# Optimization experiments

Hardware: AMD Instinct MI355X
Metric: run time of the kernel (lower is better)

Reference implementation:

```python
import jax, jax.numpy as jnp
import numpy as np

B = 262144      # batch (many robot-timestep samples)
IN_LEN = 32     # input_len
S = 64          # internal_state_len
M = 32          # message_len
P = 4           # num_ports
H = 100         # hidden_layer_size
L = 50          # lstm_hidden_size
O = 16          # output_len


def _linear_init(key, out_f, in_f):
    # torch.nn.Linear default init: U(-1/sqrt(in_f), 1/sqrt(in_f)) for W and b
    kw, kb = jax.random.split(key)
    bound = 1.0 / np.sqrt(in_f)
    W = jax.random.uniform(kw, (out_f, in_f), jnp.float32, -bound, bound)
    b = jax.random.uniform(kb, (out_f,), jnp.float32, -bound, bound)
    return W, b


def setup_inputs() -> dict:
    key = jax.random.key(0)
    ks = jax.random.split(key, 20)
    obs = jax.random.normal(ks[0], (B, IN_LEN), jnp.float32)
    messages_in = jax.random.normal(ks[1], (P, B, M), jnp.float32)
    h_lstm = jax.random.normal(ks[2], (B, L), jnp.float32)
    c_lstm = jax.random.normal(ks[3], (B, L), jnp.float32)

    W_in, b_in = _linear_init(ks[4], S, IN_LEN)
    # per-port message MLPs, stacked on a leading port axis
    msg1 = [_linear_init(jax.random.fold_in(ks[5], p), H, S) for p in range(P)]
    msg2 = [_linear_init(jax.random.fold_in(ks[6], p), M, H) for p in range(P)]
    msg_W1 = jnp.stack([w for w, _ in msg1])  # [P, H, S]
    msg_b1 = jnp.stack([b for _, b in msg1])  # [P, H]
    msg_W2 = jnp.stack([w for w, _ in msg2])  # [P, M, H]
    msg_b2 = jnp.stack([b for _, b in msg2])  # [P, M]

    # LSTMCell(S + M*P -> L); torch gate order i, f, g, o; init U(-1/sqrt(L), 1/sqrt(L))
    bl = 1.0 / np.sqrt(L)
    W_ih = jax.random.uniform(ks[7], (4 * L, S + M * P), jnp.float32, -bl, bl)
    W_hh = jax.random.uniform(ks[8], (4 * L, L), jnp.float32, -bl, bl)
    b_ih = jax.random.uniform(ks[9], (4 * L,), jnp.float32, -bl, bl)
    b_hh = jax.random.uniform(ks[10], (4 * L,), jnp.float32, -bl, bl)

    W_u1, b_u1 = _linear_init(ks[11], H, L)
    W_u2, b_u2 = _linear_init(ks[12], H, H)
    W_u3, b_u3 = _linear_init(ks[13], S, H)
    W_mu, b_mu = _linear_init(ks[14], O, S)
    W_var, b_var = _linear_init(ks[15], O, S)
    max_logvar = jnp.ones((1, O), jnp.float32) / 2.0
    min_logvar = -jnp.ones((1, O), jnp.float32) * 10.0

    return dict(obs=obs, messages_in=messages_in, h_lstm=h_lstm, c_lstm=c_lstm,
                W_in=W_in, b_in=b_in, msg_W1=msg_W1, msg_b1=msg_b1,
                msg_W2=msg_W2, msg_b2=msg_b2, W_ih=W_ih, W_hh=W_hh,
                b_ih=b_ih, b_hh=b_hh, W_u1=W_u1, b_u1=b_u1, W_u2=W_u2,
                b_u2=b_u2, W_u3=W_u3, b_u3=b_u3, W_mu=W_mu, b_mu=b_mu,
                W_var=W_var, b_var=b_var, max_logvar=max_logvar,
                min_logvar=min_logvar)


def reference(obs, messages_in, h_lstm, c_lstm, W_in, b_in, msg_W1, msg_b1,
              msg_W2, msg_b2, W_ih, W_hh, b_ih, b_hh, W_u1, b_u1, W_u2, b_u2,
              W_u3, b_u3, W_mu, b_mu, W_var, b_var, max_logvar, min_logvar):
    # run_input_function
    x = jax.nn.relu(obs @ W_in.T + b_in)                       # [B, S]

    # compute_messages_out_function: batched over ports (all ports occupied)
    m1 = jax.nn.relu(jnp.einsum('bs,phs->pbh', x, msg_W1) + msg_b1[:, None, :])
    msgs_out = jnp.einsum('pbh,pmh->pbm', m1, msg_W2) + msg_b2[:, None, :]  # [P, B, M]

    # compute_aggregation_function: concat incoming messages along feature dim
    agg = jnp.transpose(messages_in, (1, 0, 2)).reshape(obs.shape[0], -1)  # [B, P*M]
    h_mbar = jnp.concatenate([x, agg], axis=-1)                # [B, S + P*M]

    # status_update_function: one LSTMCell step (torch gate order i, f, g, o)
    gates = h_mbar @ W_ih.T + b_ih + h_lstm @ W_hh.T + b_hh    # [B, 4L]
    i, f, g, o = jnp.split(gates, 4, axis=-1)
    c_new = jax.nn.sigmoid(f) * c_lstm + jax.nn.sigmoid(i) * jnp.tanh(g)
    h_new = jax.nn.sigmoid(o) * jnp.tanh(c_new)                # [B, L]
    h2 = jax.nn.relu(h_new @ W_u1.T + b_u1)
    h2 = jax.nn.relu(h2 @ W_u2.T + b_u2)
    h2 = h2 @ W_u3.T + b_u3                                    # new internal state [B, S]

    # compute_output_function with soft logvar clamping
    mu = h2 @ W_mu.T + b_mu                                    # [B, O]
    logvar = h2 @ W_var.T + b_var
    logvar = max_logvar - jax.nn.softplus(max_logvar - logvar)
    logvar = min_logvar + jax.nn.softplus(logvar - min_logvar)
    var = jnp.exp(logvar)

    msgs_flat = jnp.transpose(msgs_out, (1, 0, 2)).reshape(obs.shape[0], -1)  # [B, P*M]
    # concat all outputs: mu(16) var(16) msgs(128) h2(64) h_new(50) c_new(50) = 324
    return jnp.concatenate([mu, var, msgs_flat, h2, h_new, c_new], axis=-1)
```

## Files before the change

kernel.cpp:

```cpp
#include <hip/hip_runtime.h>

typedef __bf16 bf16_t;
typedef __bf16 bf16x8 __attribute__((ext_vector_type(8)));
typedef float f32x4 __attribute__((ext_vector_type(4)));

#define B_TOTAL 262144
#define OUTC 324
#define ROWS 64

#define OFF_WIN   0
#define OFF_WG    2048
#define OFF_WM1   67584
#define OFF_WM2   96256
#define OFF_WU1   112640
#define OFF_WU2   119808
#define OFF_WU3   134144
#define OFF_WMV2  142336
#define BF16_TOTAL 145920

__global__ void prep_kernel(const float* W_in, const float* msg_W1, const float* msg_W2,
                            const float* W_ih, const float* W_hh, const float* b_ih, const float* b_hh,
                            const float* W_u1, const float* W_u2, const float* W_u3, const float* b_u3f,
                            const float* W_mu, const float* W_var, const float* b_mu, const float* b_var,
                            bf16_t* wb, float* bg, float* bmv) {
  int tid = blockIdx.x * blockDim.x + threadIdx.x;
  int nth = gridDim.x * blockDim.x;
  for (int i = tid; i < 2048; i += nth) wb[OFF_WIN + i] = (bf16_t)W_in[i];
  for (int i = tid; i < 65536; i += nth) {
    int n = i >> 8, k = i & 255;
    int g = n >> 6, j = n & 63;
    float v = 0.f;
    if (j < 50) {
      int r = g * 50 + j;
      if (k < 192) v = W_ih[r * 192 + k];
      else if (k < 242) v = W_hh[r * 50 + (k - 192)];
    }
    wb[OFF_WG + i] = (bf16_t)v;
  }
  for (int i = tid; i < 256; i += nth) {
    int g = i >> 6, j = i & 63;
    bg[i] = (j < 50) ? (b_ih[g * 50 + j] + b_hh[g * 50 + j]) : 0.f;
  }
  for (int i = tid; i < 4 * 112 * 64; i += nth) {
    int p = i / (112 * 64); int rem = i % (112 * 64); int n = rem >> 6, k = rem & 63;
    wb[OFF_WM1 + i] = (bf16_t)((n < 100) ? msg_W1[(p * 100 + n) * 64 + k] : 0.f);
  }
  for (int i = tid; i < 4 * 32 * 128; i += nth) {
    int p = i / (32 * 128); int rem = i % (32 * 128); int n = rem >> 7, k = rem & 127;
    wb[OFF_WM2 + i] = (bf16_t)((k < 100) ? msg_W2[(p * 32 + n) * 100 + k] : 0.f);
  }
  for (int i = tid; i < 112 * 64; i += nth) {
    int n = i >> 6, k = i & 63;
    wb[OFF_WU1 + i] = (bf16_t)((n < 100 && k < 50) ? W_u1[n * 50 + k] : 0.f);
  }
  for (int i = tid; i < 112 * 128; i += nth) {
    int n = i >> 7, k = i & 127;
    wb[OFF_WU2 + i] = (bf16_t)((n < 100 && k < 100) ? W_u2[n * 100 + k] : 0.f);
  }
  for (int i = tid; i < 64 * 128; i += nth) {
    int n = i >> 7, k = i & 127;
    wb[OFF_WU3 + i] = (bf16_t)((k < 100) ? W_u3[n * 100 + k] : 0.f);
  }
  for (int i = tid; i < 32 * 112; i += nth) {
    int o = i / 112, h = i % 112;
    float v = 0.f;
    if (h < 100) {
      const float* wrow = (o < 16) ? (W_mu + o * 64) : (W_var + (o - 16) * 64);
      for (int s = 0; s < 64; s++) v += wrow[s] * W_u3[s * 100 + h];
    }
    wb[OFF_WMV2 + i] = (bf16_t)v;
  }
  for (int i = tid; i < 32; i += nth) {
    int o = i;
    const float* wrow = (o < 16) ? (W_mu + o * 64) : (W_var + (o - 16) * 64);
    float v = (o < 16) ? b_mu[o] : b_var[o - 16];
    for (int s = 0; s < 64; s++) v += wrow[s] * b_u3f[s];
    bmv[o] = v;
  }
}

#define MFMA(a, b, c) __builtin_amdgcn_mfma_f32_16x16x32_bf16((a), (b), (c), 0, 0, 0)

__device__ __forceinline__ float frcp(float x) { return __builtin_amdgcn_rcpf(x); }
__device__ __forceinline__ float fsigmoid(float x) { return frcp(1.f + __expf(-x)); }
__device__ __forceinline__ float ftanh_f(float x) { return 1.f - 2.f * frcp(1.f + __expf(2.f * x)); }
__device__ __forceinline__ float fsoftplus(float x) { return (x > 15.f) ? x : __logf(1.f + __expf(x)); }

__device__ __forceinline__ bf16x8 cvt8(const float* __restrict__ p) {
  float4 v0 = *(const float4*)p;
  float4 v1 = *(const float4*)(p + 4);
  bf16x8 r;
  r[0] = (bf16_t)v0.x; r[1] = (bf16_t)v0.y; r[2] = (bf16_t)v0.z; r[3] = (bf16_t)v0.w;
  r[4] = (bf16_t)v1.x; r[5] = (bf16_t)v1.y; r[6] = (bf16_t)v1.z; r[7] = (bf16_t)v1.w;
  return r;
}

__device__ __forceinline__ void stage2(int p, const bf16x8 ax[4][2], bf16_t* dst,
                                       const bf16_t* __restrict__ wb,
                                       const float* __restrict__ msg_b1,
                                       int w, int lr, int kq) {
  for (int nt = w; nt < 7; nt += 4) {
    int nb = nt * 16;
    float bv = (nb + lr < 100) ? msg_b1[p * 100 + nb + lr] : 0.f;
    const bf16_t* Bp = wb + OFF_WM1 + p * 112 * 64 + (nb + lr) * 64 + kq * 8;
    bf16x8 b0 = *(const bf16x8*)Bp;
    bf16x8 b1 = *(const bf16x8*)(Bp + 32);
#pragma unroll
    for (int m = 0; m < 4; m++) {
      f32x4 acc = {bv, bv, bv, bv};
      acc = MFMA(ax[m][0], b0, acc);
      acc = MFMA(ax[m][1], b1, acc);
#pragma unroll
      for (int rr = 0; rr < 4; rr++)
        dst[(m * 16 + kq * 4 + rr) * 120 + nb + lr] = (bf16_t)fmaxf(acc[rr], 0.f);
    }
  }
}

__device__ __forceinline__ void stage3(int p, const bf16_t* src,
                                       const bf16_t* __restrict__ wb,
                                       const float* __restrict__ msg_b2,
                                       float* __restrict__ out,
                                       int row0, int w, int lr, int kq) {
  int nb = (w & 1) * 16;
  float bv = msg_b2[p * 32 + nb + lr];
  const bf16_t* Bp = wb + OFF_WM2 + p * 32 * 128 + (nb + lr) * 128 + kq * 8;
  bf16x8 b[4];
#pragma unroll
  for (int c = 0; c < 4; c++) b[c] = *(const bf16x8*)(Bp + c * 32);
#pragma unroll
  for (int mi = 0; mi < 2; mi++) {
    int m = (w >> 1) + mi * 2;
    f32x4 acc = {bv, bv, bv, bv};
#pragma unroll
    for (int c = 0; c < 4; c++) {
      bf16x8 a;
      if (c < 3) {
        a = *(const bf16x8*)(src + (m * 16 + lr) * 120 + c * 32 + kq * 8);
      } else {
        bf16x8 z = {};
        a = (kq < 2) ? *(const bf16x8*)(src + (m * 16 + lr) * 120 + 96 + kq * 8) : z;
      }
      acc = MFMA(a, b[c], acc);
    }
#pragma unroll
    for (int rr = 0; rr < 4; rr++) {
      size_t row = row0 + m * 16 + kq * 4 + rr;
      out[row * OUTC + 32 + p * 32 + nb + lr] = acc[rr];
    }
  }
}

__global__ __launch_bounds__(256, 3) void fused_kernel(
    const float* __restrict__ obs, const float* __restrict__ msg_in,
    const float* __restrict__ h_lstm, const float* __restrict__ c_lstm,
    const float* __restrict__ b_in, const float* __restrict__ msg_b1,
    const float* __restrict__ msg_b2, const float* __restrict__ b_u1,
    const float* __restrict__ b_u2, const float* __restrict__ b_u3,
    const float* __restrict__ maxlv, const float* __restrict__ minlv,
    const bf16_t* __restrict__ wb, const float* __restrict__ bg,
    const float* __restrict__ bmv, float* __restrict__ out) {
  __shared__ __align__(16) bf16_t xh[ROWS * 136];
  __shared__ __align__(16) bf16_t tA[ROWS * 120];
  __shared__ __align__(16) bf16_t tB[ROWS * 120];

  const int tid = threadIdx.x;
  const int row0 = blockIdx.x * ROWS;
  const int lane = tid & 63;
  const int w = tid >> 6;
  const int lr = lane & 15;
  const int kq = lane >> 4;

  {
    int r = tid >> 2, c0 = (tid & 3) * 16;
    const float* s = h_lstm + (size_t)(row0 + r) * 50;
    bf16x8 pk0, pk1;
#pragma unroll
    for (int q = 0; q < 8; q++) {
      int c = c0 + q;
      pk0[q] = (bf16_t)((c < 50) ? s[c] : 0.f);
    }
#pragma unroll
    for (int q = 0; q < 8; q++) {
      int c = c0 + 8 + q;
      pk1[q] = (bf16_t)((c < 50) ? s[c] : 0.f);
    }
    *(bf16x8*)(xh + r * 136 + 64 + c0) = pk0;
    *(bf16x8*)(xh + r * 136 + 64 + c0 + 8) = pk1;
  }

  {
    int nb = w * 16;
    float bv = b_in[nb + lr];
    bf16x8 b0 = *(const bf16x8*)(wb + OFF_WIN + (nb + lr) * 32 + kq * 8);
#pragma unroll
    for (int m = 0; m < 4; m++) {
      bf16x8 a0 = cvt8(obs + (size_t)(row0 + m * 16 + lr) * 32 + kq * 8);
      f32x4 acc = {bv, bv, bv, bv};
      acc = MFMA(a0, b0, acc);
#pragma unroll
      for (int rr = 0; rr < 4; rr++)
        xh[(m * 16 + kq * 4 + rr) * 136 + nb + lr] = (bf16_t)fmaxf(acc[rr], 0.f);
    }
  }
  __syncthreads();

  bf16x8 ax[4][2];
#pragma unroll
  for (int m = 0; m < 4; m++)
#pragma unroll
    for (int k = 0; k < 2; k++)
      ax[m][k] = *(const bf16x8*)(xh + (m * 16 + lr) * 136 + k * 32 + kq * 8);

  stage2(0, ax, tA, wb, msg_b1, w, lr, kq);
  __syncthreads();

  stage3(0, tA, wb, msg_b2, out, row0, w, lr, kq);
  stage2(1, ax, tB, wb, msg_b1, w, lr, kq);
  __syncthreads();
  stage3(1, tB, wb, msg_b2, out, row0, w, lr, kq);
  stage2(2, ax, tA, wb, msg_b1, w, lr, kq);
  __syncthreads();
  stage3(2, tA, wb, msg_b2, out, row0, w, lr, kq);
  stage2(3, ax, tB, wb, msg_b1, w, lr, kq);
  __syncthreads();

  {
    const int mt = w >> 1, jh = w & 1;
    const int jbase = jh * 32;
    bf16x8 m_pre[4][2];
#pragma unroll
    for (int p = 0; p < 4; p++)
#pragma unroll
      for (int ms = 0; ms < 2; ms++)
        m_pre[p][ms] = cvt8(msg_in + ((size_t)p * B_TOTAL + row0 + mt * 32 + ms * 16 + lr) * 32 + kq * 8);
    float c_pre[2][2][4];
#pragma unroll
    for (int s = 0; s < 2; s++) {
      int j = jbase + s * 16 + lr;
#pragma unroll
      for (int ms = 0; ms < 2; ms++)
#pragma unroll
        for (int rr = 0; rr < 4; rr++) {
          size_t row = row0 + mt * 32 + ms * 16 + kq * 4 + rr;
          c_pre[s][ms][rr] = (j < 50) ? c_lstm[row * 50 + j] : 0.f;
        }
    }

    stage3(3, tB, wb, msg_b2, out, row0, w, lr, kq);

    f32x4 acc[4][2][2];
#pragma unroll
    for (int g = 0; g < 4; g++)
#pragma unroll
      for (int s = 0; s < 2; s++) {
        float bb = bg[g * 64 + jbase + s * 16 + lr];
        f32x4 bi = {bb, bb, bb, bb};
        acc[g][s][0] = bi;
        acc[g][s][1] = bi;
      }
#pragma unroll
    for (int c = 0; c < 8; c++) {
      bf16x8 a[2];
#pragma unroll
      for (int ms = 0; ms < 2; ms++) {
        int row = mt * 32 + ms * 16 + lr;
        if (c < 2) {
          a[ms] = *(const bf16x8*)(xh + row * 136 + c * 32 + kq * 8);
        } else if (c < 6) {
          a[ms] = m_pre[c - 2][ms];
        } else {
          a[ms] = *(const bf16x8*)(xh + row * 136 + 64 + (c - 6) * 32 + kq * 8);
        }
      }
#pragma unroll
      for (int g = 0; g < 4; g++)
#pragma unroll
        for (int s = 0; s < 2; s++) {
          bf16x8 bfrag = *(const bf16x8*)(wb + OFF_WG +
              (size_t)(g * 64 + jbase + s * 16 + lr) * 256 + c * 32 + kq * 8);
          acc[g][s][0] = MFMA(a[0], bfrag, acc[g][s][0]);
          acc[g][s][1] = MFMA(a[1], bfrag, acc[g][s][1]);
        }
    }
#pragma unroll
    for (int s = 0; s < 2; s++) {
      int j = jbase + s * 16 + lr;
#pragma unroll
      for (int ms = 0; ms < 2; ms++) {
        int rbase = mt * 32 + ms * 16 + kq * 4;
#pragma unroll
        for (int rr = 0; rr < 4; rr++) {
          int lrow = rbase + rr;
          size_t row = row0 + lrow;
          float si = fsigmoid(acc[0][s][ms][rr]);
          float sf = fsigmoid(acc[1][s][ms][rr]);
          float gv = ftanh_f(acc[2][s][ms][rr]);
          float so = fsigmoid(acc[3][s][ms][rr]);
          float cn = sf * c_pre[s][ms][rr] + si * gv;
          float hv = so * ftanh_f(cn);
          if (j < 50) {
            out[row * OUTC + 274 + j] = cn;
            out[row * OUTC + 224 + j] = hv;
          }
          tA[lrow * 120 + j] = (bf16_t)((j < 50) ? hv : 0.f);
        }
      }
    }
  }
  __syncthreads();

  for (int nt = w; nt < 7; nt += 4) {
    int nb = nt * 16;
    float bv = (nb + lr < 100) ? b_u1[nb + lr] : 0.f;
    const bf16_t* Bp = wb + OFF_WU1 + (nb + lr) * 64 + kq * 8;
    bf16x8 b0 = *(const bf16x8*)Bp;
    bf16x8 b1 = *(const bf16x8*)(Bp + 32);
#pragma unroll
    for (int m = 0; m < 4; m++) {
      bf16x8 a0 = *(const bf16x8*)(tA + (m * 16 + lr) * 120 + kq * 8);
      bf16x8 a1 = *(const bf16x8*)(tA + (m * 16 + lr) * 120 + kq * 8 + 32);
      f32x4 acc = {bv, bv, bv, bv};
      acc = MFMA(a0, b0, acc);
      acc = MFMA(a1, b1, acc);
#pragma unroll
      for (int rr = 0; rr < 4; rr++)
        tB[(m * 16 + kq * 4 + rr) * 120 + nb + lr] = (bf16_t)fmaxf(acc[rr], 0.f);
    }
  }
  __syncthreads();

  for (int nt = w; nt < 7; nt += 4) {
    int nb = nt * 16;
    float bv = (nb + lr < 100) ? b_u2[nb + lr] : 0.f;
    const bf16_t* Bp = wb + OFF_WU2 + (nb + lr) * 128 + kq * 8;
    bf16x8 b[4];
#pragma unroll
    for (int c = 0; c < 4; c++) b[c] = *(const bf16x8*)(Bp + c * 32);
#pragma unroll
    for (int m = 0; m < 4; m++) {
      f32x4 acc = {bv, bv, bv, bv};
#pragma unroll
      for (int c = 0; c < 4; c++) {
        bf16x8 a;
        if (c < 3) {
          a = *(const bf16x8*)(tB + (m * 16 + lr) * 120 + c * 32 + kq * 8);
        } else {
          bf16x8 z = {};
          a = (kq < 2) ? *(const bf16x8*)(tB + (m * 16 + lr) * 120 + 96 + kq * 8) : z;
        }
        acc = MFMA(a, b[c], acc);
      }
#pragma unroll
      for (int rr = 0; rr < 4; rr++)
        tA[(m * 16 + kq * 4 + rr) * 120 + nb + lr] = (bf16_t)fmaxf(acc[rr], 0.f);
    }
  }
  __syncthreads();

  {
    int nb = w * 16;
    float bv = b_u3[nb + lr];
    const bf16_t* Bp = wb + OFF_WU3 + (nb + lr) * 128 + kq * 8;
    bf16x8 b[4];
#pragma unroll
    for (int c = 0; c < 4; c++) b[c] = *(const bf16x8*)(Bp + c * 32);
#pragma unroll
    for (int m = 0; m < 4; m++) {
      f32x4 acc = {bv, bv, bv, bv};
#pragma unroll
      for (int c = 0; c < 4; c++) {
        bf16x8 a;
        if (c < 3) {
          a = *(const bf16x8*)(tA + (m * 16 + lr) * 120 + c * 32 + kq * 8);
        } else {
          bf16x8 z = {};
          a = (kq < 2) ? *(const bf16x8*)(tA + (m * 16 + lr) * 120 + 96 + kq * 8) : z;
        }
        acc = MFMA(a, b[c], acc);
      }
#pragma unroll
      for (int rr = 0; rr < 4; rr++) {
        size_t row = row0 + m * 16 + kq * 4 + rr;
        out[row * OUTC + 160 + nb + lr] = acc[rr];
      }
    }
  }

  {
    int t = w & 1;
    const bf16_t* Bp = wb + OFF_WMV2 + (t * 16 + lr) * 112 + kq * 8;
    bf16x8 b[4];
#pragma unroll
    for (int c = 0; c < 3; c++) b[c] = *(const bf16x8*)(Bp + c * 32);
    {
      bf16x8 z = {};
      b[3] = (kq < 2) ? *(const bf16x8*)(Bp + 96) : z;
    }
    float bv = bmv[t * 16 + lr];
    float mx = maxlv[lr], mn = minlv[lr];
#pragma unroll
    for (int mi = 0; mi < 2; mi++) {
      int m = (w >> 1) + mi * 2;
      f32x4 acc = {bv, bv, bv, bv};
#pragma unroll
      for (int c = 0; c < 4; c++) {
        bf16x8 a;
        if (c < 3) {
          a = *(const bf16x8*)(tA + (m * 16 + lr) * 120 + c * 32 + kq * 8);
        } else {
          bf16x8 z = {};
          a = (kq < 2) ? *(const bf16x8*)(tA + (m * 16 + lr) * 120 + 96 + kq * 8) : z;
        }
        acc = MFMA(a, b[c], acc);
      }
      if (t == 0) {
#pragma unroll
        for (int rr = 0; rr < 4; rr++) {
          size_t row = row0 + m * 16 + kq * 4 + rr;
          out[row * OUTC + lr] = acc[rr];
        }
      } else {
#pragma unroll
        for (int rr = 0; rr < 4; rr++) {
          size_t row = row0 + m * 16 + kq * 4 + rr;
          float lv = acc[rr];
          lv = mx - fsoftplus(mx - lv);
          lv = mn + fsoftplus(lv - mn);
          out[row * OUTC + 16 + lr] = __expf(lv);
        }
      }
    }
  }
}

extern "C" void kernel_launch(void* const* d_in, const int* in_sizes, int n_in,
                              void* d_out, int out_size, void* d_ws, size_t ws_size,
                              hipStream_t stream) {
  const float* obs   = (const float*)d_in[0];
  const float* msgs  = (const float*)d_in[1];
  const float* h_l   = (const float*)d_in[2];
  const float* c_l   = (const float*)d_in[3];
  const float* W_in  = (const float*)d_in[4];
  const float* b_in  = (const float*)d_in[5];
  const float* mW1   = (const float*)d_in[6];
  const float* mb1   = (const float*)d_in[7];
  const float* mW2   = (const float*)d_in[8];
  const float* mb2   = (const float*)d_in[9];
  const float* W_ih  = (const float*)d_in[10];
  const float* W_hh  = (const float*)d_in[11];
  const float* b_ih  = (const float*)d_in[12];
  const float* b_hh  = (const float*)d_in[13];
  const float* W_u1  = (const float*)d_in[14];
  const float* b_u1  = (const float*)d_in[15];
  const float* W_u2  = (const float*)d_in[16];
  const float* b_u2  = (const float*)d_in[17];
  const float* W_u3  = (const float*)d_in[18];
  const float* b_u3  = (const float*)d_in[19];
  const float* W_mu  = (const float*)d_in[20];
  const float* b_mu  = (const float*)d_in[21];
  const float* W_var = (const float*)d_in[22];
  const float* b_var = (const float*)d_in[23];
  const float* maxlv = (const float*)d_in[24];
  const float* minlv = (const float*)d_in[25];

  bf16_t* wb = (bf16_t*)d_ws;
  float* bg  = (float*)((char*)d_ws + (size_t)BF16_TOTAL * 2);
  float* bmv = bg + 256;

  prep_kernel<<<64, 256, 0, stream>>>(W_in, mW1, mW2, W_ih, W_hh, b_ih, b_hh,
                                      W_u1, W_u2, W_u3, b_u3, W_mu, W_var, b_mu, b_var,
                                      wb, bg, bmv);
  fused_kernel<<<B_TOTAL / ROWS, 256, 0, stream>>>(
      obs, msgs, h_l, c_l, b_in, mb1, mb2, b_u1, b_u2, b_u3,
      maxlv, minlv, wb, bg, bmv, (float*)d_out);
}
```

Before: 355.2 us.

## Give each wave its own row slab for update MLP and defer output stores

The update MLP tail (u1, u2, u3, mu/var) now runs with each wave owning a 16-row slab and computing all output columns for it. This replaces the column split across waves and removes three block-wide barriers, with each wave's A fragments reused from registers. Message and LSTM outputs are buffered in registers and written to global memory after the LSTM stage rather than interleaved with compute. The cost is more registers per thread, which may lower occupancy under launch_bounds(256,3), and weight fragments are reloaded once per row slab.

```diff
diff --git a/kernel.cpp b/kernel.cpp
--- a/kernel.cpp
+++ b/kernel.cpp
@@ -120,8 +120,8 @@
 __device__ __forceinline__ void stage3(int p, const bf16_t* src,
                                        const bf16_t* __restrict__ wb,
                                        const float* __restrict__ msg_b2,
-                                       float* __restrict__ out,
-                                       int row0, int w, int lr, int kq) {
+                                       float (&mb)[2][4],
+                                       int w, int lr, int kq) {
   int nb = (w & 1) * 16;
   float bv = msg_b2[p * 32 + nb + lr];
   const bf16_t* Bp = wb + OFF_WM2 + p * 32 * 128 + (nb + lr) * 128 + kq * 8;
@@ -144,10 +144,7 @@
       acc = MFMA(a, b[c], acc);
     }
 #pragma unroll
-    for (int rr = 0; rr < 4; rr++) {
-      size_t row = row0 + m * 16 + kq * 4 + rr;
-      out[row * OUTC + 32 + p * 32 + nb + lr] = acc[rr];
-    }
+    for (int rr = 0; rr < 4; rr++) mb[mi][rr] = acc[rr];
   }
 }
 
@@ -171,6 +168,10 @@
   const int lr = lane & 15;
   const int kq = lane >> 4;
 
+  float mbuf[4][2][4];
+  float cnb[2][2][4];
+  float hvb[2][2][4];
+
   {
     int r = tid >> 2, c0 = (tid & 3) * 16;
     const float* s = h_lstm + (size_t)(row0 + r) * 50;
@@ -215,13 +216,13 @@
   stage2(0, ax, tA, wb, msg_b1, w, lr, kq);
   __syncthreads();
 
-  stage3(0, tA, wb, msg_b2, out, row0, w, lr, kq);
+  stage3(0, tA, wb, msg_b2, mbuf[0], w, lr, kq);
   stage2(1, ax, tB, wb, msg_b1, w, lr, kq);
   __syncthreads();
-  stage3(1, tB, wb, msg_b2, out, row0, w, lr, kq);
+  stage3(1, tB, wb, msg_b2, mbuf[1], w, lr, kq);
   stage2(2, ax, tA, wb, msg_b1, w, lr, kq);
   __syncthreads();
-  stage3(2, tA, wb, msg_b2, out, row0, w, lr, kq);
+  stage3(2, tA, wb, msg_b2, mbuf[2], w, lr, kq);
   stage2(3, ax, tB, wb, msg_b1, w, lr, kq);
   __syncthreads();
 
@@ -247,7 +248,7 @@
         }
     }
 
-    stage3(3, tB, wb, msg_b2, out, row0, w, lr, kq);
+    stage3(3, tB, wb, msg_b2, mbuf[3], w, lr, kq);
 
     f32x4 acc[4][2][2];
 #pragma unroll
@@ -292,138 +293,145 @@
 #pragma unroll
         for (int rr = 0; rr < 4; rr++) {
           int lrow = rbase + rr;
-          size_t row = row0 + lrow;
           float si = fsigmoid(acc[0][s][ms][rr]);
           float sf = fsigmoid(acc[1][s][ms][rr]);
           float gv = ftanh_f(acc[2][s][ms][rr]);
           float so = fsigmoid(acc[3][s][ms][rr]);
           float cn = sf * c_pre[s][ms][rr] + si * gv;
           float hv = so * ftanh_f(cn);
-          if (j < 50) {
-            out[row * OUTC + 274 + j] = cn;
-            out[row * OUTC + 224 + j] = hv;
+          cnb[s][ms][rr] = cn;
+          hvb[s][ms][rr] = hv;
+          tA[lrow * 120 + j] = (bf16_t)((j < 50) ? hv : 0.f);
+        }
+      }
+    }
+  }
+  __syncthreads();
+
+#pragma unroll
+  for (int p = 0; p < 4; p++) {
+    int nb = (w & 1) * 16;
+#pragma unroll
+    for (int mi = 0; mi < 2; mi++) {
+      int m = (w >> 1) + mi * 2;
+#pragma unroll
+      for (int rr = 0; rr < 4; rr++) {
+        size_t row = row0 + m * 16 + kq * 4 + rr;
+        out[row * OUTC + 32 + p * 32 + nb + lr] = mbuf[p][mi][rr];
+      }
+    }
+  }
+  {
+    const int mt = w >> 1, jh = w & 1;
+#pragma unroll
+    for (int s = 0; s < 2; s++) {
+      int j = jh * 32 + s * 16 + lr;
+      if (j < 50) {
+#pragma unroll
+        for (int ms = 0; ms < 2; ms++)
+#pragma unroll
+          for (int rr = 0; rr < 4; rr++) {
+            size_t row = row0 + mt * 32 + ms * 16 + kq * 4 + rr;
+            out[row * OUTC + 274 + j] = cnb[s][ms][rr];
+            out[row * OUTC + 224 + j] = hvb[s][ms][rr];
           }
-          tA[lrow * 120 + j] = (bf16_t)((j < 50) ? hv : 0.f);
-        }
-      }
-    }
-  }
-  __syncthreads();
-
-  for (int nt = w; nt < 7; nt += 4) {
-    int nb = nt * 16;
-    float bv = (nb + lr < 100) ? b_u1[nb + lr] : 0.f;
-    const bf16_t* Bp = wb + OFF_WU1 + (nb + lr) * 64 + kq * 8;
-    bf16x8 b0 = *(const bf16x8*)Bp;
-    bf16x8 b1 = *(const bf16x8*)(Bp + 32);
-#pragma unroll
-    for (int m = 0; m < 4; m++) {
-      bf16x8 a0 = *(const bf16x8*)(tA + (m * 16 + lr) * 120 + kq * 8);
-      bf16x8 a1 = *(const bf16x8*)(tA + (m * 16 + lr) * 120 + kq * 8 + 32);
-      f32x4 acc = {bv, bv, bv, bv};
-      acc = MFMA(a0, b0, acc);
-      acc = MFMA(a1, b1, acc);
+      }
+    }
+  }
+
+  {
+    const int LB = w * 16;
+    bf16_t* pA = tA + LB * 120;
+    bf16_t* pB = tB + LB * 120;
+    bf16x8 ah0 = *(const bf16x8*)(pA + lr * 120 + kq * 8);
+    bf16x8 ah1 = *(const bf16x8*)(pA + lr * 120 + 32 + kq * 8);
+#pragma unroll
+    for (int nt = 0; nt < 7; nt++) {
+      int nb = nt * 16;
+      float bv = (nb + lr < 100) ? b_u1[nb + lr] : 0.f;
+      const bf16_t* Bp = wb + OFF_WU1 + (nb + lr) * 64 + kq * 8;
+      bf16x8 b0 = *(const bf16x8*)Bp;
+      bf16x8 b1 = *(const bf16x8*)(Bp + 32);
+      f32x4 acc = {bv, bv, bv, bv};
+      acc = MFMA(ah0, b0, acc);
+      acc = MFMA(ah1, b1, acc);
 #pragma unroll
       for (int rr = 0; rr < 4; rr++)
-        tB[(m * 16 + kq * 4 + rr) * 120 + nb + lr] = (bf16_t)fmaxf(acc[rr], 0.f);
-    }
-  }
-  __syncthreads();
-
-  for (int nt = w; nt < 7; nt += 4) {
-    int nb = nt * 16;
-    float bv = (nb + lr < 100) ? b_u2[nb + lr] : 0.f;
-    const bf16_t* Bp = wb + OFF_WU2 + (nb + lr) * 128 + kq * 8;
-    bf16x8 b[4];
-#pragma unroll
-    for (int c = 0; c < 4; c++) b[c] = *(const bf16x8*)(Bp + c * 32);
-#pragma unroll
-    for (int m = 0; m < 4; m++) {
+        pB[(kq * 4 + rr) * 120 + nb + lr] = (bf16_t)fmaxf(acc[rr], 0.f);
+    }
+    bf16x8 a2[4];
+#pragma unroll
+    for (int c = 0; c < 3; c++) a2[c] = *(const bf16x8*)(pB + lr * 120 + c * 32 + kq * 8);
+    {
+      bf16x8 z = {};
+      a2[3] = (kq < 2) ? *(const bf16x8*)(pB + lr * 120 + 96 + kq * 8) : z;
+    }
+#pragma unroll
+    for (int nt = 0; nt < 7; nt++) {
+      int nb = nt * 16;
+      float bv = (nb + lr < 100) ? b_u2[nb + lr] : 0.f;
+      const bf16_t* Bp = wb + OFF_WU2 + (nb + lr) * 128 + kq * 8;
       f32x4 acc = {bv, bv, bv, bv};
 #pragma unroll
       for (int c = 0; c < 4; c++) {
-        bf16x8 a;
+        bf16x8 b0 = *(const bf16x8*)(Bp + c * 32);
+        acc = MFMA(a2[c], b0, acc);
+      }
+#pragma unroll
+      for (int rr = 0; rr < 4; rr++)
+        pA[(kq * 4 + rr) * 120 + nb + lr] = (bf16_t)fmaxf(acc[rr], 0.f);
+    }
+    bf16x8 a3[4];
+#pragma unroll
+    for (int c = 0; c < 3; c++) a3[c] = *(const bf16x8*)(pA + lr * 120 + c * 32 + kq * 8);
+    {
+      bf16x8 z = {};
+      a3[3] = (kq < 2) ? *(const bf16x8*)(pA + lr * 120 + 96 + kq * 8) : z;
+    }
+#pragma unroll
+    for (int nt = 0; nt < 4; nt++) {
+      int nb = nt * 16;
+      float bv = b_u3[nb + lr];
+      const bf16_t* Bp = wb + OFF_WU3 + (nb + lr) * 128 + kq * 8;
+      f32x4 acc = {bv, bv, bv, bv};
+#pragma unroll
+      for (int c = 0; c < 4; c++) {
+        bf16x8 b0 = *(const bf16x8*)(Bp + c * 32);
+        acc = MFMA(a3[c], b0, acc);
+      }
+#pragma unroll
+      for (int rr = 0; rr < 4; rr++) {
+        size_t row = row0 + LB + kq * 4 + rr;
+        out[row * OUTC + 160 + nb + lr] = acc[rr];
+      }
+    }
+    float mx = maxlv[lr], mn = minlv[lr];
+#pragma unroll
+    for (int t = 0; t < 2; t++) {
+      float bv = bmv[t * 16 + lr];
+      const bf16_t* Bp = wb + OFF_WMV2 + (t * 16 + lr) * 112 + kq * 8;
+      f32x4 acc = {bv, bv, bv, bv};
+#pragma unroll
+      for (int c = 0; c < 4; c++) {
+        bf16x8 b0;
         if (c < 3) {
-          a = *(const bf16x8*)(tB + (m * 16 + lr) * 120 + c * 32 + kq * 8);
+          b0 = *(const bf16x8*)(Bp + c * 32);
         } else {
           bf16x8 z = {};
-          a = (kq < 2) ? *(const bf16x8*)(tB + (m * 16 + lr) * 120 + 96 + kq * 8) : z;
-        }
-        acc = MFMA(a, b[c], acc);
-      }
-#pragma unroll
-      for (int rr = 0; rr < 4; rr++)
-        tA[(m * 16 + kq * 4 + rr) * 120 + nb + lr] = (bf16_t)fmaxf(acc[rr], 0.f);
-    }
-  }
-  __syncthreads();
-
-  {
-    int nb = w * 16;
-    float bv = b_u3[nb + lr];
-    const bf16_t* Bp = wb + OFF_WU3 + (nb + lr) * 128 + kq * 8;
-    bf16x8 b[4];
-#pragma unroll
-    for (int c = 0; c < 4; c++) b[c] = *(const bf16x8*)(Bp + c * 32);
-#pragma unroll
-    for (int m = 0; m < 4; m++) {
-      f32x4 acc = {bv, bv, bv, bv};
-#pragma unroll
-      for (int c = 0; c < 4; c++) {
-        bf16x8 a;
-        if (c < 3) {
-          a = *(const bf16x8*)(tA + (m * 16 + lr) * 120 + c * 32 + kq * 8);
-        } else {
-          bf16x8 z = {};
-          a = (kq < 2) ? *(const bf16x8*)(tA + (m * 16 + lr) * 120 + 96 + kq * 8) : z;
-        }
-        acc = MFMA(a, b[c], acc);
-      }
-#pragma unroll
-      for (int rr = 0; rr < 4; rr++) {
-        size_t row = row0 + m * 16 + kq * 4 + rr;
-        out[row * OUTC + 160 + nb + lr] = acc[rr];
-      }
-    }
-  }
-
-  {
-    int t = w & 1;
-    const bf16_t* Bp = wb + OFF_WMV2 + (t * 16 + lr) * 112 + kq * 8;
-    bf16x8 b[4];
-#pragma unroll
-    for (int c = 0; c < 3; c++) b[c] = *(const bf16x8*)(Bp + c * 32);
-    {
-      bf16x8 z = {};
-      b[3] = (kq < 2) ? *(const bf16x8*)(Bp + 96) : z;
-    }
-    float bv = bmv[t * 16 + lr];
-    float mx = maxlv[lr], mn = minlv[lr];
-#pragma unroll
-    for (int mi = 0; mi < 2; mi++) {
-      int m = (w >> 1) + mi * 2;
-      f32x4 acc = {bv, bv, bv, bv};
-#pragma unroll
-      for (int c = 0; c < 4; c++) {
-        bf16x8 a;
-        if (c < 3) {
-          a = *(const bf16x8*)(tA + (m * 16 + lr) * 120 + c * 32 + kq * 8);
-        } else {
-          bf16x8 z = {};
-          a = (kq < 2) ? *(const bf16x8*)(tA + (m * 16 + lr) * 120 + 96 + kq * 8) : z;
-        }
-        acc = MFMA(a, b[c], acc);
+          b0 = (kq < 2) ? *(const bf16x8*)(Bp + 96) : z;
+        }
+        acc = MFMA(a3[c], b0, acc);
       }
       if (t == 0) {
 #pragma unroll
         for (int rr = 0; rr < 4; rr++) {
-          size_t row = row0 + m * 16 + kq * 4 + rr;
+          size_t row = row0 + LB + kq * 4 + rr;
           out[row * OUTC + lr] = acc[rr];
         }
       } else {
 #pragma unroll
         for (int rr = 0; rr < 4; rr++) {
-          size_t row = row0 + m * 16 + kq * 4 + rr;
+          size_t row = row0 + LB + kq * 4 + rr;
           float lv = acc[rr];
           lv = mx - fsoftplus(mx - lv);
           lv = mn + fsoftplus(lv - mn);
```

Result: slower. 481.7 us (+35.6%).
